# Performance work log

Hardware: AMD Instinct MI355X
Metric: run time of the kernel (lower is better)

The kernel has to match this reference:

```python
import jax, jax.numpy as jnp
import numpy as np

B, S, ED, H, L = 128, 100, 1024, 16, 48
D = ED // H      # head dim = 64
M = 1024 // H    # per-head mapping dim = 64
SIGMA = 2.0 ** -100  # 1 / 2**seq_len with seq_len=100


def _phi(xh, W):
    # xh: [B,S,H,D], W: [H,M,D] -> [B,S,H,M]
    norm_x = jnp.linalg.norm(xh)
    proj = jnp.einsum('hmd,bshd->bshm', W, xh)
    return jnp.exp(proj) * jnp.exp(-norm_x ** 2 / 2) / M


def setup_inputs() -> dict:
    key = jax.random.key(0)
    ks = jax.random.split(key, 10)
    x = jax.random.normal(ks[0], (B, S, ED), dtype=jnp.float32)
    sc = 1.0 / np.sqrt(ED)
    Wq = jax.random.uniform(ks[1], (ED, ED), jnp.float32, -sc, sc)
    Wk = jax.random.uniform(ks[2], (ED, ED), jnp.float32, -sc, sc)
    Wv = jax.random.uniform(ks[3], (ED, ED), jnp.float32, -sc, sc)
    bq = jax.random.uniform(ks[4], (ED,), jnp.float32, -sc, sc)
    bk = jax.random.uniform(ks[5], (ED,), jnp.float32, -sc, sc)
    bv = jax.random.uniform(ks[6], (ED,), jnp.float32, -sc, sc)
    # Linformer buffers: R row-normalized, E = sigma*R, F = exp(-sigma)*R
    R = jax.random.normal(ks[7], (S, L), dtype=jnp.float32) / np.sqrt(L)
    R = R / jnp.clip(jnp.linalg.norm(R, axis=1, keepdims=True), 1e-12)
    E = jnp.float32(SIGMA) * R
    F = jnp.exp(jnp.float32(-SIGMA)) * R
    # random-feature projection weights [H, M, D]
    Wrf = jax.random.normal(ks[8], (H, M, D), dtype=jnp.float32)
    return {'x': x, 'Wq': Wq, 'bq': bq, 'Wk': Wk, 'bk': bk, 'Wv': Wv,
            'bv': bv, 'Wrf': Wrf, 'E': E, 'F': F}


def reference(x, Wq, bq, Wk, bk, Wv, bv, Wrf, E, F):
    b, s, _ = x.shape
    q = (x @ Wq.T + bq).reshape(b, s, H, D)
    k = (x @ Wk.T + bk).reshape(b, s, H, D)
    v = (x @ Wv.T + bv).reshape(b, s, H, D)
    # global (whole-tensor) normalization, as in the torch code
    q = q / jnp.linalg.norm(q)
    k = k / jnp.linalg.norm(k)
    phi_q = jnp.transpose(_phi(q, Wrf), (0, 2, 1, 3))  # [B,H,S,M]
    phi_k = jnp.transpose(_phi(k, Wrf), (0, 2, 1, 3))  # [B,H,S,M]
    A2 = phi_k
    phi_k_l = jnp.einsum('bhsm,sl->bhlm', phi_k, E)     # [B,H,L,M]
    v_l = jnp.einsum('bshd,sl->blhd', v, F)             # [B,L,H,D]
    v_l = jnp.transpose(v_l, (0, 2, 1, 3))              # [B,H,L,D]
    A1 = jnp.einsum('bhlm,bhld->bhmd', phi_k_l, v_l)    # [B,H,M,D]
    num = jnp.einsum('bhsm,bhmd->bhsd', phi_q, A1)      # [B,H,S,D]
    den = jnp.einsum('bhsm,bhsm->bhs', phi_q, A2)[..., None]
    out = num / den
    return jnp.transpose(out, (0, 2, 1, 3)).reshape(b, s, ED)
```

## Files before the change

### kernel.cpp

```cpp
#include <hip/hip_runtime.h>
#include <math.h>

#define BQ 128
#define SQ 100
#define HH 16
#define LL 48
#define BS (BQ*SQ)

typedef __bf16 bf16_t;
typedef bf16_t bf16x8 __attribute__((ext_vector_type(8)));
typedef float f32x4 __attribute__((ext_vector_type(4)));

#define QBH_OFF  0ull
#define KBH_OFF  26214400ull
#define VT_OFF   52428800ull
#define XB_OFF   85983232ull
#define PHQ_OFF  85983232ull
#define WB_OFF   112197632ull
#define WRFB_OFF 118489088ull
#define G_OFF    118620160ull
#define PHK_OFF  118648832ull
#define SC_OFF   197292032ull

__device__ __forceinline__ void gload16(const bf16_t* g, bf16_t* l) {
    __builtin_amdgcn_global_load_lds(
        (const __attribute__((address_space(1))) void*)g,
        (__attribute__((address_space(3))) void*)l, 16, 0, 0);
}

__global__ __launch_bounds__(256)
void kprep(const float* __restrict__ x, const float* __restrict__ Wq,
           const float* __restrict__ Wk, const float* __restrict__ Wv,
           const float* __restrict__ Wrf, const float* __restrict__ E,
           const float* __restrict__ F,
           bf16_t* __restrict__ xb, bf16_t* __restrict__ wb,
           bf16_t* __restrict__ wrfb, bf16_t* __restrict__ G,
           bf16_t* __restrict__ vt, float* __restrict__ sc) {
    const int bid = blockIdx.x;
    const int tid = threadIdx.x;
    if (bid < 1024) {
        const f32x4* x4 = (const f32x4*)x;
        for (int i = bid*256 + tid; i < BS*1024/4; i += 1024*256) {
            f32x4 v = x4[i];
            bf16_t* o = xb + 4*(size_t)i;
            o[0]=(bf16_t)v[0]; o[1]=(bf16_t)v[1]; o[2]=(bf16_t)v[2]; o[3]=(bf16_t)v[3];
        }
    } else if (bid < 1536) {
        for (int i = (bid-1024)*256 + tid; i < 3*1024*1024/4; i += 512*256) {
            const int f = i*4;
            const int row = f >> 10;
            const int col = f & 1023;
            const float* src = (row < 1024) ? Wq : ((row < 2048) ? Wk : Wv);
            const f32x4 v = *(const f32x4*)(src + ((size_t)(row & 1023) << 10) + col);
            bf16_t* o = wb + (size_t)f;
            o[0]=(bf16_t)v[0]; o[1]=(bf16_t)v[1]; o[2]=(bf16_t)v[2]; o[3]=(bf16_t)v[3];
        }
    } else if (bid < 1792) {
        for (int i = (bid-1536)*256 + tid; i < 131072*14; i += 256*256) {
            const int row = i / 14, dw = i - row*14;
            ((unsigned int*)((char*)vt + (size_t)row*256 + 200))[dw] = 0u;
        }
    } else if (bid < 1856) {
        const int i = (bid-1792)*256 + tid;
        const f32x4 v = ((const f32x4*)Wrf)[i];
        bf16_t* p = wrfb + 4*(size_t)i;
        p[0]=(bf16_t)v[0]; p[1]=(bf16_t)v[1]; p[2]=(bf16_t)v[2]; p[3]=(bf16_t)v[3];
    } else if (bid < 1912) {
        const int idx = (bid-1856)*256 + tid;
        const int s = idx >> 7, t = idx & 127;
        float acc = 0.f;
        if (s < 100 && t < 100) {
#pragma unroll
            for (int l = 0; l < LL; l++) acc += E[s*LL+l]*F[t*LL+l];
        }
        G[idx] = (bf16_t)acc;
    } else {
        if (tid < 4) sc[tid] = 0.f;
    }
}

__global__ __launch_bounds__(256)
void kgemm(const bf16_t* __restrict__ xb, const bf16_t* __restrict__ wb,
           const float* __restrict__ bq, const float* __restrict__ bk,
           const float* __restrict__ bv,
           bf16_t* __restrict__ qbh, bf16_t* __restrict__ kbh,
           bf16_t* __restrict__ vt, float* __restrict__ ssq) {
    __shared__ __align__(16) bf16_t smem[24576];
    bf16_t* sA = smem;
    bf16_t* sB = smem + 12288;
    const int lane = threadIdx.x & 63;
    const int wid  = threadIdx.x >> 6;
    const int row0 = blockIdx.y * 128;
    const int col0 = blockIdx.x * 128;
    const int wr = (wid >> 1) * 64;
    const int wc = (wid & 1) * 64;
    const int ar = lane & 15;
    const int kg = lane >> 4;

    const int srow = lane >> 2;
    const int sslot = (lane & 3) ^ ((lane >> 3) & 3);
    const int scol = sslot * 8;
    const bf16_t* gA0 = xb + (size_t)(row0 + wid*16 + srow) * 1024 + scol;
    const bf16_t* gA1 = gA0 + (size_t)64 * 1024;
    const bf16_t* gB0 = wb + (size_t)(col0 + wid*16 + srow) * 1024 + scol;
    const bf16_t* gB1 = gB0 + (size_t)64 * 1024;
    const int lOffA0 = (wid*16) * 32;
    const int lOffA1 = (64 + wid*16) * 32;

    const int aslot = (kg ^ ((ar >> 1) & 3)) * 8;

    f32x4 acc[4][4];
#pragma unroll
    for (int m = 0; m < 4; m++)
#pragma unroll
        for (int n = 0; n < 4; n++)
            acc[m][n] = (f32x4){0.f, 0.f, 0.f, 0.f};

#define STAGE(buf, t) do { const int kk_ = (t)*32; \
        gload16(gA0 + kk_, sA + (buf)*4096 + lOffA0); \
        gload16(gA1 + kk_, sA + (buf)*4096 + lOffA1); \
        gload16(gB0 + kk_, sB + (buf)*4096 + lOffA0); \
        gload16(gB1 + kk_, sB + (buf)*4096 + lOffA1); } while(0)

    STAGE(0, 0);
    STAGE(1, 1);

    for (int ks = 0; ks < 32; ks++) {
        if (ks < 31) asm volatile("s_waitcnt vmcnt(4)" ::: "memory");
        else         asm volatile("s_waitcnt vmcnt(0)" ::: "memory");
        __builtin_amdgcn_sched_barrier(0);
        __builtin_amdgcn_s_barrier();
        __builtin_amdgcn_sched_barrier(0);
        const int p = ks % 3;
        if (ks + 2 < 32) {
            const int nb = (ks + 2) % 3;
            STAGE(nb, ks + 2);
        }
        bf16x8 a[4], bb[4];
#pragma unroll
        for (int rf = 0; rf < 4; rf++)
            a[rf] = *(const bf16x8*)&sA[p*4096 + (wr + rf*16 + ar)*32 + aslot];
#pragma unroll
        for (int cf = 0; cf < 4; cf++)
            bb[cf] = *(const bf16x8*)&sB[p*4096 + (wc + cf*16 + ar)*32 + aslot];
#pragma unroll
        for (int rf = 0; rf < 4; rf++)
#pragma unroll
            for (int cf = 0; cf < 4; cf++)
                acc[rf][cf] = __builtin_amdgcn_mfma_f32_16x16x32_bf16(
                    a[rf], bb[cf], acc[rf][cf], 0, 0, 0);
    }
#undef STAGE

    const int which = col0 >> 10;
    const int cc0 = col0 & 1023;

    __syncthreads();

    float ss = 0.f;
    if (which < 2) {
#pragma unroll
        for (int n = 0; n < 4; n++) {
            const float bias = (which == 0 ? bq : bk)[cc0 + wc + n*16 + ar];
            const int c = wc + n*16 + ar;
#pragma unroll
            for (int m = 0; m < 4; m++) {
#pragma unroll
                for (int j = 0; j < 4; j++) {
                    const int r = wr + m*16 + kg*4 + j;
                    const float val = acc[m][n][j] + bias;
                    ss += val * val;
                    smem[r*128 + (c ^ ((r&7)<<3))] = (bf16_t)val;
                }
            }
        }
    } else {
#pragma unroll
        for (int n = 0; n < 4; n++) {
            const float bias = bv[cc0 + wc + n*16 + ar];
            const int c = wc + n*16 + ar;
#pragma unroll
            for (int m = 0; m < 4; m++) {
#pragma unroll
                for (int j = 0; j < 4; j++) {
                    const int r = wr + m*16 + kg*4 + j;
                    const float val = acc[m][n][j] + bias;
                    smem[c*128 + (r ^ ((c&7)<<3))] = (bf16_t)val;
                }
            }
        }
    }
    __syncthreads();

    if (which < 2) {
        bf16_t* ob = (which == 0) ? qbh : kbh;
#pragma unroll
        for (int i = 0; i < 8; i++) {
            const int e = i*2048 + threadIdx.x*8;
            const int r = e >> 7;
            const int c0 = e & 127;
            const bf16x8 chunk = *(const bf16x8*)&smem[r*128 + (c0 ^ ((r&7)<<3))];
            *(bf16x8*)(ob + (size_t)(row0 + r)*1024 + cc0 + c0) = chunk;
        }
        for (int off = 32; off; off >>= 1) ss += __shfl_xor(ss, off);
        if (lane == 0 && ss != 0.f) atomicAdd(ssq + which, ss);
    } else {
#pragma unroll
        for (int i = 0; i < 8; i++) {
            const int e = i*2048 + threadIdx.x*8;
            const int c = e >> 7;
            const int r0 = e & 127;
            const bf16x8 chunk = *(const bf16x8*)&smem[c*128 + (r0 ^ ((c&7)<<3))];
            const int cc = cc0 + c;
            const int h2 = cc >> 6, d = cc & 63;
            const int rg = row0 + r0;
            const int b2 = rg / 100;
            const int s2 = rg - b2*100;
            if (s2 <= 92) {
                *(bf16x8*)(vt + ((size_t)(b2*16 + h2)*64 + d)*128 + s2) = chunk;
            } else {
#pragma unroll
                for (int t = 0; t < 8; t++) {
                    const int rgt = rg + t;
                    const int b3 = rgt / 100;
                    const int s3 = rgt - b3*100;
                    vt[((size_t)(b3*16 + h2)*64 + d)*128 + s3] = chunk[t];
                }
            }
        }
    }
}

__global__ __launch_bounds__(256)
void kphi_mfma(const bf16_t* __restrict__ qbh, const bf16_t* __restrict__ kbh,
               const bf16_t* __restrict__ wrfb, const float* __restrict__ sc,
               bf16_t* __restrict__ phqb, bf16_t* __restrict__ phkb) {
    __shared__ __align__(16) bf16_t sT[4 * 2 * 16 * 72];
    const int lane = threadIdx.x & 63;
    const int wid  = threadIdx.x >> 6;
    const int h    = blockIdx.y;
    const int bs0  = blockIdx.x * 256 + wid * 64;
    const int ar = lane & 15;
    const int kg = lane >> 4;
    bf16_t* tq = sT + wid * 2304;
    bf16_t* tk = tq + 1152;

    bf16x8 bfr[4][2];
#pragma unroll
    for (int cf = 0; cf < 4; cf++)
#pragma unroll
        for (int ks = 0; ks < 2; ks++)
            bfr[cf][ks] = *(const bf16x8*)(wrfb +
                ((size_t)(h * 64 + cf * 16 + ar) * 64 + ks * 32 + kg * 8));

    f32x4 aq[4][4], ak[4][4];
#pragma unroll
    for (int rf = 0; rf < 4; rf++)
#pragma unroll
        for (int cf = 0; cf < 4; cf++) {
            aq[rf][cf] = (f32x4){0.f, 0.f, 0.f, 0.f};
            ak[rf][cf] = (f32x4){0.f, 0.f, 0.f, 0.f};
        }

#pragma unroll
    for (int rf = 0; rf < 4; rf++) {
        const size_t urow = ((size_t)(bs0 + rf*16 + ar) * 16 + h) * 64 + kg * 8;
        const bf16x8 a0 = *(const bf16x8*)(qbh + urow);
        const bf16x8 a1 = *(const bf16x8*)(qbh + urow + 32);
        const bf16x8 c0 = *(const bf16x8*)(kbh + urow);
        const bf16x8 c1 = *(const bf16x8*)(kbh + urow + 32);
#pragma unroll
        for (int cf = 0; cf < 4; cf++) {
            aq[rf][cf] = __builtin_amdgcn_mfma_f32_16x16x32_bf16(a0, bfr[cf][0], aq[rf][cf], 0, 0, 0);
            aq[rf][cf] = __builtin_amdgcn_mfma_f32_16x16x32_bf16(a1, bfr[cf][1], aq[rf][cf], 0, 0, 0);
            ak[rf][cf] = __builtin_amdgcn_mfma_f32_16x16x32_bf16(c0, bfr[cf][0], ak[rf][cf], 0, 0, 0);
            ak[rf][cf] = __builtin_amdgcn_mfma_f32_16x16x32_bf16(c1, bfr[cf][1], ak[rf][cf], 0, 0, 0);
        }
    }

    const float qs  = rsqrtf(sc[0]);
    const float ksc = rsqrtf(sc[1]);
    const float CPHI = 0.009477041545882225f;

    const int rl0 = lane >> 3;
    const int ce0 = (lane & 7) * 8;

    for (int rf = 0; rf < 4; rf++) {
        float t[4] = {0.f, 0.f, 0.f, 0.f};
        float vq[4][4], vk[4][4];
#pragma unroll
        for (int cf = 0; cf < 4; cf++) {
#pragma unroll
            for (int j = 0; j < 4; j++) {
                const float q_ = expf(aq[rf][cf][j] * qs) * CPHI;
                const float k_ = expf(ak[rf][cf][j] * ksc) * CPHI;
                vq[cf][j] = q_;
                vk[cf][j] = k_;
                t[j] += q_ * k_;
            }
        }
#pragma unroll
        for (int j = 0; j < 4; j++) {
            t[j] += __shfl_xor(t[j], 1);
            t[j] += __shfl_xor(t[j], 2);
            t[j] += __shfl_xor(t[j], 4);
            t[j] += __shfl_xor(t[j], 8);
            t[j] = 1.0f / t[j];
        }
#pragma unroll
        for (int cf = 0; cf < 4; cf++) {
#pragma unroll
            for (int j = 0; j < 4; j++) {
                const int rr = kg*4 + j;
                tq[rr*72 + cf*16 + ar] = (bf16_t)(vq[cf][j] * t[j]);
                tk[rr*72 + cf*16 + ar] = (bf16_t)vk[cf][j];
            }
        }
        asm volatile("s_waitcnt lgkmcnt(0)" ::: "memory");
        __builtin_amdgcn_sched_barrier(0);
#pragma unroll
        for (int half = 0; half < 2; half++) {
            const int rl = rl0 + half*8;
            const int bs = bs0 + rf*16 + rl;
            const int b = bs / 100;
            const int s = bs - b * 100;
            const size_t o = (((size_t)b*16 + h)*100 + s)*64 + ce0;
            *(bf16x8*)(phqb + o) = *(const bf16x8*)&tq[rl*72 + ce0];
            *(bf16x8*)(phkb + o) = *(const bf16x8*)&tk[rl*72 + ce0];
        }
        asm volatile("s_waitcnt lgkmcnt(0)" ::: "memory");
        __builtin_amdgcn_sched_barrier(0);
    }
}

__global__ __launch_bounds__(256)
void kPnum(const bf16_t* __restrict__ phq, const bf16_t* __restrict__ phk,
           const bf16_t* __restrict__ vt, const bf16_t* __restrict__ G,
           float* __restrict__ out) {
    __shared__ bf16_t sP[112 * 128];
    __shared__ bf16_t sW[64 * 128];
    const int lane = threadIdx.x & 63;
    const int w    = threadIdx.x >> 6;
    const int bh   = blockIdx.x;
    const int b = bh >> 4, h = bh & 15;
    const int ar = lane & 15;
    const int kg = lane >> 4;
    const bf16_t* qb = phq + (size_t)bh * 6400;
    const bf16_t* kb = phk + (size_t)bh * 6400;

    {
        const bf16_t* vb = vt + (size_t)bh * 8192;
        bf16x8 a[4];
#pragma unroll
        for (int ks = 0; ks < 4; ks++)
            a[ks] = *(const bf16x8*)(vb + (w*16 + ar)*128 + ks*32 + kg*8);

#pragma unroll
        for (int cf = 0; cf < 7; cf++) {
            f32x4 acc = (f32x4){0.f,0.f,0.f,0.f};
#pragma unroll
            for (int ks = 0; ks < 4; ks++) {
                const bf16x8 bb = *(const bf16x8*)(G + (cf*16 + ar)*128 + ks*32 + kg*8);
                acc = __builtin_amdgcn_mfma_f32_16x16x32_bf16(a[ks], bb, acc, 0, 0, 0);
            }
#pragma unroll
            for (int j = 0; j < 4; j++) {
                const int d = w*16 + kg*4 + j;
                const int sp = cf*16 + ar;
                sW[d*128 + (sp ^ ((d&7)<<3))] = (bf16_t)acc[j];
            }
        }
#pragma unroll
        for (int j = 0; j < 4; j++) {
            const int d = w*16 + kg*4 + j;
            sW[d*128 + ((112 + ar) ^ ((d&7)<<3))] = (bf16_t)0.f;
        }
    }

    bf16x8 bfr[7][2];
#pragma unroll
    for (int cf = 0; cf < 7; cf++) {
        int sp = cf*16 + ar; sp = sp > 99 ? 99 : sp;
#pragma unroll
        for (int ks = 0; ks < 2; ks++)
            bfr[cf][ks] = *(const bf16x8*)(kb + sp*64 + ks*32 + kg*8);
    }

#pragma unroll
    for (int rr = 0; rr < 2; rr++) {
        const int rf = w + rr*4;
        if (rf > 6) continue;
        int s = rf*16 + ar; s = s > 99 ? 99 : s;
        const bf16x8 a0 = *(const bf16x8*)(qb + s*64 + kg*8);
        const bf16x8 a1 = *(const bf16x8*)(qb + s*64 + 32 + kg*8);
        f32x4 acc[7];
#pragma unroll
        for (int cf = 0; cf < 7; cf++) acc[cf] = (f32x4){0.f,0.f,0.f,0.f};
#pragma unroll
        for (int cf = 0; cf < 7; cf++) {
            acc[cf] = __builtin_amdgcn_mfma_f32_16x16x32_bf16(a0, bfr[cf][0], acc[cf], 0, 0, 0);
            acc[cf] = __builtin_amdgcn_mfma_f32_16x16x32_bf16(a1, bfr[cf][1], acc[cf], 0, 0, 0);
        }
#pragma unroll
        for (int cf = 0; cf < 7; cf++) {
#pragma unroll
            for (int j = 0; j < 4; j++) {
                const int so = rf*16 + kg*4 + j;
                const int sp = cf*16 + ar;
                if (so < 100)
                    sP[so*128 + (sp ^ ((so&7)<<3))] =
                        (bf16_t)(sp < 100 ? acc[cf][j] : 0.f);
            }
        }
#pragma unroll
        for (int j = 0; j < 4; j++) {
            const int so = rf*16 + kg*4 + j;
            if (so < 100) {
                const int sp = 112 + ar;
                sP[so*128 + (sp ^ ((so&7)<<3))] = (bf16_t)0.f;
            }
        }
    }
    __syncthreads();

    bf16x8 wfr[4][4];
#pragma unroll
    for (int cf = 0; cf < 4; cf++) {
        const int d = cf*16 + ar;
#pragma unroll
        for (int ks = 0; ks < 4; ks++)
            wfr[cf][ks] = *(const bf16x8*)&sW[d*128 + ((ks*32 + kg*8) ^ ((d&7)<<3))];
    }

#pragma unroll
    for (int rr = 0; rr < 2; rr++) {
        const int rf = w + rr*4;
        if (rf > 6) continue;
        int s = rf*16 + ar; s = s > 99 ? 99 : s;
        bf16x8 a[4];
#pragma unroll
        for (int ks = 0; ks < 4; ks++)
            a[ks] = *(const bf16x8*)&sP[s*128 + ((ks*32 + kg*8) ^ ((s&7)<<3))];
        f32x4 acc[4];
#pragma unroll
        for (int cf = 0; cf < 4; cf++) acc[cf] = (f32x4){0.f,0.f,0.f,0.f};
#pragma unroll
        for (int cf = 0; cf < 4; cf++)
#pragma unroll
            for (int ks = 0; ks < 4; ks++)
                acc[cf] = __builtin_amdgcn_mfma_f32_16x16x32_bf16(a[ks], wfr[cf][ks], acc[cf], 0, 0, 0);
#pragma unroll
        for (int cf = 0; cf < 4; cf++) {
#pragma unroll
            for (int j = 0; j < 4; j++) {
                const int so = rf*16 + kg*4 + j;
                if (so < 100)
                    out[((size_t)(b*100 + so)*16 + h)*64 + cf*16 + ar] = acc[cf][j];
            }
        }
    }
}

extern "C" void kernel_launch(void* const* d_in, const int* in_sizes, int n_in,
                              void* d_out, int out_size, void* d_ws, size_t ws_size,
                              hipStream_t stream) {
    const float* x   = (const float*)d_in[0];
    const float* Wq  = (const float*)d_in[1];
    const float* bq  = (const float*)d_in[2];
    const float* Wk  = (const float*)d_in[3];
    const float* bk  = (const float*)d_in[4];
    const float* Wv  = (const float*)d_in[5];
    const float* bv  = (const float*)d_in[6];
    const float* Wrf = (const float*)d_in[7];
    const float* E   = (const float*)d_in[8];
    const float* F   = (const float*)d_in[9];
    float* out = (float*)d_out;

    char* ws = (char*)d_ws;
    bf16_t* qbh  = (bf16_t*)(ws + QBH_OFF);
    bf16_t* kbh  = (bf16_t*)(ws + KBH_OFF);
    bf16_t* vt   = (bf16_t*)(ws + VT_OFF);
    bf16_t* xb   = (bf16_t*)(ws + XB_OFF);
    bf16_t* phqb = (bf16_t*)(ws + PHQ_OFF);
    bf16_t* wb   = (bf16_t*)(ws + WB_OFF);
    bf16_t* wrfb = (bf16_t*)(ws + WRFB_OFF);
    bf16_t* G    = (bf16_t*)(ws + G_OFF);
    bf16_t* phkb = (bf16_t*)(ws + PHK_OFF);
    float*  sc   = (float*)(ws + SC_OFF);

    kprep<<<1913, 256, 0, stream>>>(x, Wq, Wk, Wv, Wrf, E, F,
                                    xb, wb, wrfb, G, vt, sc);

    dim3 ggrid(24, 100);
    kgemm<<<ggrid, 256, 0, stream>>>(xb, wb, bq, bk, bv, qbh, kbh, vt, sc);

    dim3 pgrid(50, 16);
    kphi_mfma<<<pgrid, 256, 0, stream>>>(qbh, kbh, wrfb, sc, phqb, phkb);

    kPnum<<<BQ * HH, 256, 0, stream>>>(phqb, phkb, vt, G, out);
}
```

Measured before the change: 237.4 us.

## Fuse random-feature phi computation into per-(batch,head) attention kernel

Merges the phi kernel and the P/num kernel into one per-(b,h) kernel. Each block computes phi_q (normalized by its denominator) and phi_k for its 100 rows into shared memory and feeds them straight into the QK^T-like product, with the LDS pool reused for the V/G product. This removes the bf16 phi_q/phi_k round trip through global memory and one kernel launch. In exchange shared memory use rises to about 60KB per block, which may lower occupancy, and the phi work is now spread over 2048 blocks with 7 row tiles each.

```diff
diff --git a/kernel.cpp b/kernel.cpp
--- a/kernel.cpp
+++ b/kernel.cpp
@@ -15,11 +15,9 @@
 #define KBH_OFF  26214400ull
 #define VT_OFF   52428800ull
 #define XB_OFF   85983232ull
-#define PHQ_OFF  85983232ull
 #define WB_OFF   112197632ull
 #define WRFB_OFF 118489088ull
 #define G_OFF    118620160ull
-#define PHK_OFF  118648832ull
 #define SC_OFF   197292032ull
 
 __device__ __forceinline__ void gload16(const bf16_t* g, bf16_t* l) {
@@ -232,121 +230,139 @@
 }
 
 __global__ __launch_bounds__(256)
-void kphi_mfma(const bf16_t* __restrict__ qbh, const bf16_t* __restrict__ kbh,
-               const bf16_t* __restrict__ wrfb, const float* __restrict__ sc,
-               bf16_t* __restrict__ phqb, bf16_t* __restrict__ phkb) {
-    __shared__ __align__(16) bf16_t sT[4 * 2 * 16 * 72];
-    const int lane = threadIdx.x & 63;
-    const int wid  = threadIdx.x >> 6;
-    const int h    = blockIdx.y;
-    const int bs0  = blockIdx.x * 256 + wid * 64;
-    const int ar = lane & 15;
-    const int kg = lane >> 4;
-    bf16_t* tq = sT + wid * 2304;
-    bf16_t* tk = tq + 1152;
-
-    bf16x8 bfr[4][2];
-#pragma unroll
-    for (int cf = 0; cf < 4; cf++)
-#pragma unroll
-        for (int ks = 0; ks < 2; ks++)
-            bfr[cf][ks] = *(const bf16x8*)(wrfb +
-                ((size_t)(h * 64 + cf * 16 + ar) * 64 + ks * 32 + kg * 8));
-
-    f32x4 aq[4][4], ak[4][4];
-#pragma unroll
-    for (int rf = 0; rf < 4; rf++)
-#pragma unroll
-        for (int cf = 0; cf < 4; cf++) {
-            aq[rf][cf] = (f32x4){0.f, 0.f, 0.f, 0.f};
-            ak[rf][cf] = (f32x4){0.f, 0.f, 0.f, 0.f};
-        }
-
-#pragma unroll
-    for (int rf = 0; rf < 4; rf++) {
-        const size_t urow = ((size_t)(bs0 + rf*16 + ar) * 16 + h) * 64 + kg * 8;
-        const bf16x8 a0 = *(const bf16x8*)(qbh + urow);
-        const bf16x8 a1 = *(const bf16x8*)(qbh + urow + 32);
-        const bf16x8 c0 = *(const bf16x8*)(kbh + urow);
-        const bf16x8 c1 = *(const bf16x8*)(kbh + urow + 32);
-#pragma unroll
-        for (int cf = 0; cf < 4; cf++) {
-            aq[rf][cf] = __builtin_amdgcn_mfma_f32_16x16x32_bf16(a0, bfr[cf][0], aq[rf][cf], 0, 0, 0);
-            aq[rf][cf] = __builtin_amdgcn_mfma_f32_16x16x32_bf16(a1, bfr[cf][1], aq[rf][cf], 0, 0, 0);
-            ak[rf][cf] = __builtin_amdgcn_mfma_f32_16x16x32_bf16(c0, bfr[cf][0], ak[rf][cf], 0, 0, 0);
-            ak[rf][cf] = __builtin_amdgcn_mfma_f32_16x16x32_bf16(c1, bfr[cf][1], ak[rf][cf], 0, 0, 0);
-        }
-    }
-
-    const float qs  = rsqrtf(sc[0]);
-    const float ksc = rsqrtf(sc[1]);
-    const float CPHI = 0.009477041545882225f;
-
-    const int rl0 = lane >> 3;
-    const int ce0 = (lane & 7) * 8;
-
-    for (int rf = 0; rf < 4; rf++) {
-        float t[4] = {0.f, 0.f, 0.f, 0.f};
-        float vq[4][4], vk[4][4];
-#pragma unroll
-        for (int cf = 0; cf < 4; cf++) {
-#pragma unroll
-            for (int j = 0; j < 4; j++) {
-                const float q_ = expf(aq[rf][cf][j] * qs) * CPHI;
-                const float k_ = expf(ak[rf][cf][j] * ksc) * CPHI;
-                vq[cf][j] = q_;
-                vk[cf][j] = k_;
-                t[j] += q_ * k_;
-            }
-        }
-#pragma unroll
-        for (int j = 0; j < 4; j++) {
-            t[j] += __shfl_xor(t[j], 1);
-            t[j] += __shfl_xor(t[j], 2);
-            t[j] += __shfl_xor(t[j], 4);
-            t[j] += __shfl_xor(t[j], 8);
-            t[j] = 1.0f / t[j];
-        }
-#pragma unroll
-        for (int cf = 0; cf < 4; cf++) {
-#pragma unroll
-            for (int j = 0; j < 4; j++) {
-                const int rr = kg*4 + j;
-                tq[rr*72 + cf*16 + ar] = (bf16_t)(vq[cf][j] * t[j]);
-                tk[rr*72 + cf*16 + ar] = (bf16_t)vk[cf][j];
-            }
-        }
-        asm volatile("s_waitcnt lgkmcnt(0)" ::: "memory");
-        __builtin_amdgcn_sched_barrier(0);
-#pragma unroll
-        for (int half = 0; half < 2; half++) {
-            const int rl = rl0 + half*8;
-            const int bs = bs0 + rf*16 + rl;
-            const int b = bs / 100;
-            const int s = bs - b * 100;
-            const size_t o = (((size_t)b*16 + h)*100 + s)*64 + ce0;
-            *(bf16x8*)(phqb + o) = *(const bf16x8*)&tq[rl*72 + ce0];
-            *(bf16x8*)(phkb + o) = *(const bf16x8*)&tk[rl*72 + ce0];
-        }
-        asm volatile("s_waitcnt lgkmcnt(0)" ::: "memory");
-        __builtin_amdgcn_sched_barrier(0);
-    }
-}
-
-__global__ __launch_bounds__(256)
-void kPnum(const bf16_t* __restrict__ phq, const bf16_t* __restrict__ phk,
-           const bf16_t* __restrict__ vt, const bf16_t* __restrict__ G,
-           float* __restrict__ out) {
-    __shared__ bf16_t sP[112 * 128];
-    __shared__ bf16_t sW[64 * 128];
+void kfused(const bf16_t* __restrict__ qbh, const bf16_t* __restrict__ kbh,
+            const bf16_t* __restrict__ wrfb, const float* __restrict__ sc,
+            const bf16_t* __restrict__ vt, const bf16_t* __restrict__ G,
+            float* __restrict__ out) {
+    __shared__ __align__(16) char pool[60928];
+    bf16_t* tQ = (bf16_t*)pool;
+    bf16_t* tK = (bf16_t*)(pool + 16128);
+    bf16_t* sP = (bf16_t*)(pool + 32256);
+    bf16_t* sW = (bf16_t*)pool;
+
     const int lane = threadIdx.x & 63;
     const int w    = threadIdx.x >> 6;
     const int bh   = blockIdx.x;
     const int b = bh >> 4, h = bh & 15;
     const int ar = lane & 15;
     const int kg = lane >> 4;
-    const bf16_t* qb = phq + (size_t)bh * 6400;
-    const bf16_t* kb = phk + (size_t)bh * 6400;
+
+    {
+        bf16x8 bfr[4][2];
+#pragma unroll
+        for (int cf = 0; cf < 4; cf++)
+#pragma unroll
+            for (int ks = 0; ks < 2; ks++)
+                bfr[cf][ks] = *(const bf16x8*)(wrfb +
+                    ((size_t)(h * 64 + cf * 16 + ar) * 64 + ks * 32 + kg * 8));
+
+        const float qs  = rsqrtf(sc[0]);
+        const float ksc = rsqrtf(sc[1]);
+        const float CPHI = 0.009477041545882225f;
+
+#pragma unroll
+        for (int rr = 0; rr < 2; rr++) {
+            const int rf = w + rr*4;
+            if (rf > 6) continue;
+            int s_src = rf*16 + ar; s_src = s_src > 99 ? 99 : s_src;
+            const size_t urow = ((size_t)(b*100 + s_src) * 16 + h) * 64 + kg * 8;
+            const bf16x8 a0 = *(const bf16x8*)(qbh + urow);
+            const bf16x8 a1 = *(const bf16x8*)(qbh + urow + 32);
+            const bf16x8 c0 = *(const bf16x8*)(kbh + urow);
+            const bf16x8 c1 = *(const bf16x8*)(kbh + urow + 32);
+            f32x4 aq[4], ak[4];
+#pragma unroll
+            for (int cf = 0; cf < 4; cf++) {
+                aq[cf] = (f32x4){0.f,0.f,0.f,0.f};
+                ak[cf] = (f32x4){0.f,0.f,0.f,0.f};
+            }
+#pragma unroll
+            for (int cf = 0; cf < 4; cf++) {
+                aq[cf] = __builtin_amdgcn_mfma_f32_16x16x32_bf16(a0, bfr[cf][0], aq[cf], 0, 0, 0);
+                aq[cf] = __builtin_amdgcn_mfma_f32_16x16x32_bf16(a1, bfr[cf][1], aq[cf], 0, 0, 0);
+                ak[cf] = __builtin_amdgcn_mfma_f32_16x16x32_bf16(c0, bfr[cf][0], ak[cf], 0, 0, 0);
+                ak[cf] = __builtin_amdgcn_mfma_f32_16x16x32_bf16(c1, bfr[cf][1], ak[cf], 0, 0, 0);
+            }
+            float t[4] = {0.f,0.f,0.f,0.f};
+            float vq[4][4], vk[4][4];
+#pragma unroll
+            for (int cf = 0; cf < 4; cf++) {
+#pragma unroll
+                for (int j = 0; j < 4; j++) {
+                    const float q_ = expf(aq[cf][j] * qs) * CPHI;
+                    const float k_ = expf(ak[cf][j] * ksc) * CPHI;
+                    vq[cf][j] = q_;
+                    vk[cf][j] = k_;
+                    t[j] += q_ * k_;
+                }
+            }
+#pragma unroll
+            for (int j = 0; j < 4; j++) {
+                t[j] += __shfl_xor(t[j], 1);
+                t[j] += __shfl_xor(t[j], 2);
+                t[j] += __shfl_xor(t[j], 4);
+                t[j] += __shfl_xor(t[j], 8);
+                t[j] = 1.0f / t[j];
+            }
+#pragma unroll
+            for (int cf = 0; cf < 4; cf++) {
+#pragma unroll
+                for (int j = 0; j < 4; j++) {
+                    const int rr2 = rf*16 + kg*4 + j;
+                    tQ[rr2*72 + cf*16 + ar] = (bf16_t)(vq[cf][j] * t[j]);
+                    tK[rr2*72 + cf*16 + ar] = (bf16_t)vk[cf][j];
+                }
+            }
+        }
+    }
+    __syncthreads();
+
+    {
+        bf16x8 bfr[7][2];
+#pragma unroll
+        for (int cf = 0; cf < 7; cf++) {
+            const int sp = cf*16 + ar;
+#pragma unroll
+            for (int ks = 0; ks < 2; ks++)
+                bfr[cf][ks] = *(const bf16x8*)&tK[sp*72 + ks*32 + kg*8];
+        }
+#pragma unroll
+        for (int rr = 0; rr < 2; rr++) {
+            const int rf = w + rr*4;
+            if (rf > 6) continue;
+            const int s = rf*16 + ar;
+            const bf16x8 a0 = *(const bf16x8*)&tQ[s*72 + kg*8];
+            const bf16x8 a1 = *(const bf16x8*)&tQ[s*72 + 32 + kg*8];
+            f32x4 acc[7];
+#pragma unroll
+            for (int cf = 0; cf < 7; cf++) acc[cf] = (f32x4){0.f,0.f,0.f,0.f};
+#pragma unroll
+            for (int cf = 0; cf < 7; cf++) {
+                acc[cf] = __builtin_amdgcn_mfma_f32_16x16x32_bf16(a0, bfr[cf][0], acc[cf], 0, 0, 0);
+                acc[cf] = __builtin_amdgcn_mfma_f32_16x16x32_bf16(a1, bfr[cf][1], acc[cf], 0, 0, 0);
+            }
+#pragma unroll
+            for (int cf = 0; cf < 7; cf++) {
+#pragma unroll
+                for (int j = 0; j < 4; j++) {
+                    const int so = rf*16 + kg*4 + j;
+                    const int sp = cf*16 + ar;
+                    if (so < 100)
+                        sP[so*128 + (sp ^ ((so&7)<<3))] =
+                            (bf16_t)(sp < 100 ? acc[cf][j] : 0.f);
+                }
+            }
+#pragma unroll
+            for (int j = 0; j < 4; j++) {
+                const int so = rf*16 + kg*4 + j;
+                if (so < 100) {
+                    const int sp = 112 + ar;
+                    sP[so*128 + (sp ^ ((so&7)<<3))] = (bf16_t)0.f;
+                }
+            }
+        }
+    }
+    __syncthreads();
 
     {
         const bf16_t* vb = vt + (size_t)bh * 8192;
@@ -376,86 +392,42 @@
             sW[d*128 + ((112 + ar) ^ ((d&7)<<3))] = (bf16_t)0.f;
         }
     }
-
-    bf16x8 bfr[7][2];
-#pragma unroll
-    for (int cf = 0; cf < 7; cf++) {
-        int sp = cf*16 + ar; sp = sp > 99 ? 99 : sp;
-#pragma unroll
-        for (int ks = 0; ks < 2; ks++)
-            bfr[cf][ks] = *(const bf16x8*)(kb + sp*64 + ks*32 + kg*8);
-    }
-
-#pragma unroll
-    for (int rr = 0; rr < 2; rr++) {
-        const int rf = w + rr*4;
-        if (rf > 6) continue;
-        int s = rf*16 + ar; s = s > 99 ? 99 : s;
-        const bf16x8 a0 = *(const bf16x8*)(qb + s*64 + kg*8);
-        const bf16x8 a1 = *(const bf16x8*)(qb + s*64 + 32 + kg*8);
-        f32x4 acc[7];
-#pragma unroll
-        for (int cf = 0; cf < 7; cf++) acc[cf] = (f32x4){0.f,0.f,0.f,0.f};
-#pragma unroll
-        for (int cf = 0; cf < 7; cf++) {
-            acc[cf] = __builtin_amdgcn_mfma_f32_16x16x32_bf16(a0, bfr[cf][0], acc[cf], 0, 0, 0);
-            acc[cf] = __builtin_amdgcn_mfma_f32_16x16x32_bf16(a1, bfr[cf][1], acc[cf], 0, 0, 0);
-        }
-#pragma unroll
-        for (int cf = 0; cf < 7; cf++) {
-#pragma unroll
-            for (int j = 0; j < 4; j++) {
-                const int so = rf*16 + kg*4 + j;
-                const int sp = cf*16 + ar;
-                if (so < 100)
-                    sP[so*128 + (sp ^ ((so&7)<<3))] =
-                        (bf16_t)(sp < 100 ? acc[cf][j] : 0.f);
-            }
-        }
-#pragma unroll
-        for (int j = 0; j < 4; j++) {
-            const int so = rf*16 + kg*4 + j;
-            if (so < 100) {
-                const int sp = 112 + ar;
-                sP[so*128 + (sp ^ ((so&7)<<3))] = (bf16_t)0.f;
-            }
-        }
-    }
     __syncthreads();
 
-    bf16x8 wfr[4][4];
-#pragma unroll
-    for (int cf = 0; cf < 4; cf++) {
-        const int d = cf*16 + ar;
-#pragma unroll
-        for (int ks = 0; ks < 4; ks++)
-            wfr[cf][ks] = *(const bf16x8*)&sW[d*128 + ((ks*32 + kg*8) ^ ((d&7)<<3))];
-    }
-
-#pragma unroll
-    for (int rr = 0; rr < 2; rr++) {
-        const int rf = w + rr*4;
-        if (rf > 6) continue;
-        int s = rf*16 + ar; s = s > 99 ? 99 : s;
-        bf16x8 a[4];
-#pragma unroll
-        for (int ks = 0; ks < 4; ks++)
-            a[ks] = *(const bf16x8*)&sP[s*128 + ((ks*32 + kg*8) ^ ((s&7)<<3))];
-        f32x4 acc[4];
-#pragma unroll
-        for (int cf = 0; cf < 4; cf++) acc[cf] = (f32x4){0.f,0.f,0.f,0.f};
-#pragma unroll
-        for (int cf = 0; cf < 4; cf++)
+    {
+        bf16x8 wfr[4][4];
+#pragma unroll
+        for (int cf = 0; cf < 4; cf++) {
+            const int d = cf*16 + ar;
 #pragma unroll
             for (int ks = 0; ks < 4; ks++)
-                acc[cf] = __builtin_amdgcn_mfma_f32_16x16x32_bf16(a[ks], wfr[cf][ks], acc[cf], 0, 0, 0);
-#pragma unroll
-        for (int cf = 0; cf < 4; cf++) {
-#pragma unroll
-            for (int j = 0; j < 4; j++) {
-                const int so = rf*16 + kg*4 + j;
-                if (so < 100)
-                    out[((size_t)(b*100 + so)*16 + h)*64 + cf*16 + ar] = acc[cf][j];
+                wfr[cf][ks] = *(const bf16x8*)&sW[d*128 + ((ks*32 + kg*8) ^ ((d&7)<<3))];
+        }
+#pragma unroll
+        for (int rr = 0; rr < 2; rr++) {
+            const int rf = w + rr*4;
+            if (rf > 6) continue;
+            int s = rf*16 + ar; s = s > 99 ? 99 : s;
+            bf16x8 a[4];
+#pragma unroll
+            for (int ks = 0; ks < 4; ks++)
+                a[ks] = *(const bf16x8*)&sP[s*128 + ((ks*32 + kg*8) ^ ((s&7)<<3))];
+            f32x4 acc[4];
+#pragma unroll
+            for (int cf = 0; cf < 4; cf++) acc[cf] = (f32x4){0.f,0.f,0.f,0.f};
+#pragma unroll
+            for (int cf = 0; cf < 4; cf++)
+#pragma unroll
+                for (int ks = 0; ks < 4; ks++)
+                    acc[cf] = __builtin_amdgcn_mfma_f32_16x16x32_bf16(a[ks], wfr[cf][ks], acc[cf], 0, 0, 0);
+#pragma unroll
+            for (int cf = 0; cf < 4; cf++) {
+#pragma unroll
+                for (int j = 0; j < 4; j++) {
+                    const int so = rf*16 + kg*4 + j;
+                    if (so < 100)
+                        out[((size_t)(b*100 + so)*16 + h)*64 + cf*16 + ar] = acc[cf][j];
+                }
             }
         }
     }
@@ -481,11 +453,9 @@
     bf16_t* kbh  = (bf16_t*)(ws + KBH_OFF);
     bf16_t* vt   = (bf16_t*)(ws + VT_OFF);
     bf16_t* xb   = (bf16_t*)(ws + XB_OFF);
-    bf16_t* phqb = (bf16_t*)(ws + PHQ_OFF);
     bf16_t* wb   = (bf16_t*)(ws + WB_OFF);
     bf16_t* wrfb = (bf16_t*)(ws + WRFB_OFF);
     bf16_t* G    = (bf16_t*)(ws + G_OFF);
-    bf16_t* phkb = (bf16_t*)(ws + PHK_OFF);
     float*  sc   = (float*)(ws + SC_OFF);
 
     kprep<<<1913, 256, 0, stream>>>(x, Wq, Wk, Wv, Wrf, E, F,
@@ -494,8 +464,5 @@
     dim3 ggrid(24, 100);
     kgemm<<<ggrid, 256, 0, stream>>>(xb, wb, bq, bk, bv, qbh, kbh, vt, sc);
 
-    dim3 pgrid(50, 16);
-    kphi_mfma<<<pgrid, 256, 0, stream>>>(qbh, kbh, wrfb, sc, phqb, phkb);
-
-    kPnum<<<BQ * HH, 256, 0, stream>>>(phqb, phkb, vt, G, out);
+    kfused<<<BQ * HH, 256, 0, stream>>>(qbh, kbh, wrfb, sc, vt, G, out);
 }
```

Result: faster. 211.9 us, median of 2 (-10.7%).
